# Kernel tuning notes

Measured on AMD Instinct MI355X. Metric: run time of the kernel, lower is better.

## Reference

```python
import jax, jax.numpy as jnp
import numpy as np

B, T, V, E, H, O = 32, 512, 32000, 512, 1024, 128


def setup_inputs() -> dict:
    key = jax.random.key(0)
    ks = jax.random.split(key, 8)
    s = lambda k, shape: (jax.random.normal(k, shape) * 0.02).astype(jnp.float32)
    return {
        "tokens": jax.random.randint(ks[0], (B, T), 0, V),
        "verb_indices": jax.random.randint(ks[1], (B,), 0, T),
        "emb": s(ks[2], (V, E)),
        "W_ih": s(ks[3], (4 * H, E)),
        "W_hh": s(ks[4], (4 * H, H)),
        "b_ih": jnp.zeros((4 * H,), jnp.float32),
        "b_hh": jnp.zeros((4 * H,), jnp.float32),
        "W_lin": s(ks[5], (O, 2 * H)),
        "b_lin": jnp.zeros((O,), jnp.float32),
    }


def _lstm(e, W_ih, W_hh, b_ih, b_hh):
    # e: [B,T,E] -> hidden states [B,T,H]; PyTorch gate order i,f,g,o
    Hd = W_hh.shape[1]
    # precompute input projections for all timesteps (one big GEMM)
    x_proj = jnp.einsum("bte,ge->btg", e, W_ih) + b_ih + b_hh  # [B,T,4H]

    def step(carry, x_t):
        h, c = carry
        gates = x_t + h @ W_hh.T  # [B,4H]
        i, f, g, o = jnp.split(gates, 4, axis=-1)
        i = jax.nn.sigmoid(i)
        f = jax.nn.sigmoid(f)
        g = jnp.tanh(g)
        o = jax.nn.sigmoid(o)
        c = f * c + i * g
        h = o * jnp.tanh(c)
        return (h, c), h

    h0 = jnp.zeros((e.shape[0], Hd), e.dtype)
    (_, _), hs = jax.lax.scan(step, (h0, h0), jnp.swapaxes(x_proj, 0, 1))
    return jnp.swapaxes(hs, 0, 1)  # [B,T,H]


def reference(tokens, verb_indices, emb, W_ih, W_hh, b_ih, b_hh, W_lin, b_lin):
    e = emb[tokens]  # [B,T,E]
    out = _lstm(e, W_ih, W_hh, b_ih, b_hh)  # [B,T,H]
    verbs = out[jnp.arange(out.shape[0]), verb_indices]  # [B,H] verb hidden state
    # linear over concat([verb, out_t]) == split the weight and sum two GEMMs
    Wv, Wo = jnp.split(W_lin, 2, axis=1)  # [O,H] each
    logits = (
        jnp.einsum("bh,oh->bo", verbs, Wv)[:, None, :]
        + jnp.einsum("bth,oh->bto", out, Wo)
        + b_lin
    )  # [B,T,O]
    return jax.nn.log_softmax(logits, axis=-1)
```

## Files before the change

### kernel.cpp

```cpp
#include <hip/hip_runtime.h>


typedef short s8v __attribute__((ext_vector_type(8)));
typedef float f4v __attribute__((ext_vector_type(4)));
typedef unsigned int u4v __attribute__((ext_vector_type(4)));

#define WS_CNT_OFF   131072
#define WS_VROWS_OFF 139264
#define WS_VLOG_OFF  204800

__device__ __forceinline__ float b2f(unsigned short u) {
    union { unsigned int i; float f; } x; x.i = ((unsigned int)u) << 16; return x.f;
}
__device__ __forceinline__ unsigned short f2b(float f) {
    union { float f; unsigned int i; } x; x.f = f;
    unsigned int r = (x.i + 0x7fffu + ((x.i >> 16) & 1u)) >> 16;
    return (unsigned short)r;
}
__device__ __forceinline__ float blo(unsigned int u) {
    union { unsigned int i; float f; } x; x.i = u << 16; return x.f;
}
__device__ __forceinline__ float bhi(unsigned int u) {
    union { unsigned int i; float f; } x; x.i = u & 0xffff0000u; return x.f;
}

__global__ void init_kernel(unsigned int* ws) {
    int i = blockIdx.x * 256 + threadIdx.x;
    if (i < 34816) ws[i] = 0u;
}

__device__ __forceinline__ void project_cols(
    const short* hA, const float* __restrict__ Wr0, const float* __restrict__ Wr1,
    float* __restrict__ dout, int b0, int tproj, int w, int tid)
{
    const int pair = tid >> 4, p = tid & 15;
    const int b = pair >> 1, oc = pair & 1;
    const float* wr = oc ? Wr1 : Wr0;
    float acc = 0.f;
#pragma unroll
    for (int j = 0; j < 8; ++j) {
        int ko = j * 16 + p;
        u4v d = *(const u4v*)&hA[(ko * 17 + b) * 8];
        const float* wk = wr + ko * 8;
        f4v w0 = *(const f4v*)wk, w1 = *(const f4v*)(wk + 4);
        unsigned int d0 = d[0], d1 = d[1], d2 = d[2], d3 = d[3];
        acc += blo(d0) * w0[0] + bhi(d0) * w0[1] + blo(d1) * w0[2] + bhi(d1) * w0[3]
             + blo(d2) * w1[0] + bhi(d2) * w1[1] + blo(d3) * w1[2] + bhi(d3) * w1[3];
    }
#pragma unroll
    for (int off = 1; off < 16; off <<= 1) acc += __shfl_xor(acc, off);
    if (p == 0)
        dout[((size_t)(b0 + b) * 512 + tproj) * 128 + 2 * w + oc] = acc;
}

__global__ __launch_bounds__(256, 1) void scan_kernel(
    const int* __restrict__ tokens,
    const int* __restrict__ vidx,
    const float* __restrict__ emb,
    const float* __restrict__ W_ih,
    const float* __restrict__ W_hh,
    const float* __restrict__ b_ih,
    const float* __restrict__ b_hh,
    const float* __restrict__ W_lin,
    unsigned short* __restrict__ hbuf,
    unsigned int* __restrict__ flags_all,
    unsigned short* __restrict__ vrows,
    float* __restrict__ dout)
{
    __shared__ short hA[128 * 17 * 8];
    __shared__ short eA[64 * 17 * 8];
    __shared__ float gbuf[16 * 65];

    const int tid  = threadIdx.x;
    const int g    = blockIdx.x >> 6;
    const int w    = blockIdx.x & 63;
    const int b0   = g * 8;
    const int lane = tid & 63;
    const int v    = tid >> 6;
    const int q    = lane >> 4;
    const int c    = lane & 15;

    const float* Wr0 = W_lin + (size_t)(2 * w) * 2048 + 1024;
    const float* Wr1 = W_lin + (size_t)(2 * w + 1) * 2048 + 1024;

    const int n = ((c >> 2) * 1024) + 16 * w + 4 * v + (c & 3);
    s8v Bh[32], Be[16];
    {
        const float* rh = W_hh + (size_t)n * 1024;
#pragma unroll
        for (int ks = 0; ks < 32; ++ks) {
            const float* s = rh + ks * 32 + q * 8;
            f4v lo = *(const f4v*)s, hi = *(const f4v*)(s + 4);
            s8v f;
#pragma unroll
            for (int j = 0; j < 4; ++j) { f[j] = (short)f2b(lo[j]); f[j + 4] = (short)f2b(hi[j]); }
            Bh[ks] = f;
        }
        const float* re = W_ih + (size_t)n * 512;
#pragma unroll
        for (int ks = 0; ks < 16; ++ks) {
            const float* s = re + ks * 32 + q * 8;
            f4v lo = *(const f4v*)s, hi = *(const f4v*)(s + 4);
            s8v f;
#pragma unroll
            for (int j = 0; j < 4; ++j) { f[j] = (short)f2b(lo[j]); f[j + 4] = (short)f2b(hi[j]); }
            Be[ks] = f;
        }
    }

    const s8v zv = {0,0,0,0,0,0,0,0};
    for (int i = tid; i < 1024; i += 256) { int ko = i >> 3, r = 8 + (i & 7);
        *(s8v*)&hA[(ko * 17 + r) * 8] = zv; }
    for (int i = tid; i < 512; i += 256) { int ko = i >> 3, r = 8 + (i & 7);
        *(s8v*)&eA[(ko * 17 + r) * 8] = zv; }

    float cst0 = 0.f, cst1 = 0.f;
    float bi0 = 0, bf0 = 0, bg0 = 0, bo0 = 0, bi1 = 0, bf1 = 0, bg1 = 0, bo1 = 0;
    int tvb = -1;
    const int pb = tid >> 3, pj2 = tid & 7;
    if (tid < 64) {
        int n0 = 16 * w + 2 * pj2, n1 = n0 + 1;
        bi0 = b_ih[n0]        + b_hh[n0];        bi1 = b_ih[n1]        + b_hh[n1];
        bf0 = b_ih[1024 + n0] + b_hh[1024 + n0]; bf1 = b_ih[1024 + n1] + b_hh[1024 + n1];
        bg0 = b_ih[2048 + n0] + b_hh[2048 + n0]; bg1 = b_ih[2048 + n1] + b_hh[2048 + n1];
        bo0 = b_ih[3072 + n0] + b_hh[3072 + n0]; bo1 = b_ih[3072 + n1] + b_hh[3072 + n1];
        tvb = vidx[b0 + pb];
    }

    unsigned short* hb   = hbuf + g * 2 * 8192;
    unsigned int*   hb32 = (unsigned int*)hb;
    unsigned int*   gflags = flags_all + g * 128;
    const int dwidx = ((2 * w + (pj2 >> 2)) * 8 + pb) * 4 + (pj2 & 3);
    int rp = 0;
    __syncthreads();

    for (int t = 0; t < 512; ++t) {
        for (int i = tid; i < 512; i += 256) {
            int ko = i >> 3, b = i & 7;
            int tok = tokens[(b0 + b) * 512 + t];
            const float* s = emb + (size_t)tok * 512 + ko * 8;
            f4v lo = *(const f4v*)s, hi = *(const f4v*)(s + 4);
            s8v f;
#pragma unroll
            for (int j = 0; j < 4; ++j) { f[j] = (short)f2b(lo[j]); f[j + 4] = (short)f2b(hi[j]); }
            *(s8v*)&eA[(ko * 17 + b) * 8] = f;
        }

        if (t >= 2)
            project_cols(hA, Wr0, Wr1, dout, b0, t - 2, w, tid);

        __syncthreads();

        f4v ae = {0.f, 0.f, 0.f, 0.f};
#pragma unroll
        for (int ks = 0; ks < 16; ++ks) {
            s8v a = *(const s8v*)&eA[((ks * 4 + q) * 17 + c) * 8];
            ae = __builtin_amdgcn_mfma_f32_16x16x32_bf16(a, Be[ks], ae, 0, 0, 0);
        }

        if (t > 0) {
            const unsigned tt = (unsigned)t;
            for (;;) {
                unsigned f = __hip_atomic_load(&gflags[lane], __ATOMIC_RELAXED,
                                               __HIP_MEMORY_SCOPE_AGENT);
                if (__all(f >= tt)) break;
            }
            asm volatile("" ::: "memory");
        }

        {
            const unsigned long long* src =
                (const unsigned long long*)(hb + rp * 8192);
#pragma unroll
            for (int it = 0; it < 8; ++it) {
                int j = it * 256 + tid;
                unsigned long long d = __hip_atomic_load(src + j, __ATOMIC_RELAXED,
                                                         __HIP_MEMORY_SCOPE_AGENT);
                int ko = j >> 4, b = (j >> 1) & 7, posq = (j & 1) << 2;
                *(unsigned long long*)&hA[(ko * 17 + b) * 8 + posq] = d;
            }
        }
        __syncthreads();

        f4v ah0 = {0.f, 0.f, 0.f, 0.f}, ah1 = {0.f, 0.f, 0.f, 0.f};
#pragma unroll
        for (int ks = 0; ks < 16; ++ks) {
            s8v a0 = *(const s8v*)&hA[((2 * ks) * 4 + q) * 17 * 8 + c * 8];
            s8v a1 = *(const s8v*)&hA[((2 * ks + 1) * 4 + q) * 17 * 8 + c * 8];
            ah0 = __builtin_amdgcn_mfma_f32_16x16x32_bf16(a0, Bh[2 * ks], ah0, 0, 0, 0);
            ah1 = __builtin_amdgcn_mfma_f32_16x16x32_bf16(a1, Bh[2 * ks + 1], ah1, 0, 0, 0);
        }

#pragma unroll
        for (int r = 0; r < 4; ++r)
            gbuf[(q * 4 + r) * 65 + v * 16 + c] = ae[r] + ah0[r] + ah1[r];
        __syncthreads();

        if (tid < 64) {
            float h0, h1;
            {
                int pj = 2 * pj2, base = (pj >> 2) * 16, cb = pj & 3;
                float xi = gbuf[pb * 65 + base + cb]      + bi0;
                float xf = gbuf[pb * 65 + base + 4 + cb]  + bf0;
                float xg = gbuf[pb * 65 + base + 8 + cb]  + bg0;
                float xo = gbuf[pb * 65 + base + 12 + cb] + bo0;
                float ig = 1.f / (1.f + __expf(-xi));
                float fg = 1.f / (1.f + __expf(-xf));
                float gg = 1.f - 2.f / (1.f + __expf(2.f * xg));
                float og = 1.f / (1.f + __expf(-xo));
                cst0 = fg * cst0 + ig * gg;
                h0 = og * (1.f - 2.f / (1.f + __expf(2.f * cst0)));
            }
            {
                int pj = 2 * pj2 + 1, base = (pj >> 2) * 16, cb = pj & 3;
                float xi = gbuf[pb * 65 + base + cb]      + bi1;
                float xf = gbuf[pb * 65 + base + 4 + cb]  + bf1;
                float xg = gbuf[pb * 65 + base + 8 + cb]  + bg1;
                float xo = gbuf[pb * 65 + base + 12 + cb] + bo1;
                float ig = 1.f / (1.f + __expf(-xi));
                float fg = 1.f / (1.f + __expf(-xf));
                float gg = 1.f - 2.f / (1.f + __expf(2.f * xg));
                float og = 1.f / (1.f + __expf(-xo));
                cst1 = fg * cst1 + ig * gg;
                h1 = og * (1.f - 2.f / (1.f + __expf(2.f * cst1)));
            }
            unsigned int pack = (unsigned int)f2b(h0) | ((unsigned int)f2b(h1) << 16);
            __hip_atomic_store(&hb32[(rp ^ 1) * 4096 + dwidx], pack,
                               __ATOMIC_RELAXED, __HIP_MEMORY_SCOPE_AGENT);
            if (t == tvb)
                *(unsigned int*)&vrows[(b0 + pb) * 1024 + 16 * w + 2 * pj2] = pack;
            asm volatile("s_waitcnt vmcnt(0)" ::: "memory");
            if (tid == 0)
                __hip_atomic_store(&gflags[w], (unsigned)(t + 1),
                                   __ATOMIC_RELAXED, __HIP_MEMORY_SCOPE_AGENT);
        }
        rp ^= 1;
    }

    project_cols(hA, Wr0, Wr1, dout, b0, 510, w, tid);
    __syncthreads();
    for (;;) {
        unsigned f = __hip_atomic_load(&gflags[lane], __ATOMIC_RELAXED,
                                       __HIP_MEMORY_SCOPE_AGENT);
        if (__all(f >= 512u)) break;
    }
    asm volatile("" ::: "memory");
    {
        const unsigned long long* src = (const unsigned long long*)(hb + rp * 8192);
#pragma unroll
        for (int it = 0; it < 8; ++it) {
            int j = it * 256 + tid;
            unsigned long long d = __hip_atomic_load(src + j, __ATOMIC_RELAXED,
                                                     __HIP_MEMORY_SCOPE_AGENT);
            int ko = j >> 4, b = (j >> 1) & 7, posq = (j & 1) << 2;
            *(unsigned long long*)&hA[(ko * 17 + b) * 8 + posq] = d;
        }
    }
    __syncthreads();
    project_cols(hA, Wr0, Wr1, dout, b0, 511, w, tid);
}

__global__ void verb_kernel(const unsigned short* __restrict__ vrows,
                            const float* __restrict__ W_lin,
                            const float* __restrict__ b_lin,
                            float* __restrict__ vlog)
{
    __shared__ float vrow[1024];
    int b = blockIdx.x, tid = threadIdx.x;
    for (int i = tid; i < 1024; i += 256) vrow[i] = b2f(vrows[b * 1024 + i]);
    __syncthreads();
    if (tid < 128) {
        float acc = 0.f;
        const float* wr = W_lin + (size_t)tid * 2048;
        for (int h = 0; h < 1024; ++h) acc += vrow[h] * wr[h];
        vlog[b * 128 + tid] = acc + b_lin[tid];
    }
}

__global__ void softmax_kernel(float* __restrict__ dout,
                               const float* __restrict__ vlog)
{
    int tid = threadIdx.x;
    int grow = blockIdx.x * 32 + (tid >> 3);
    int part = tid & 7;
    int b = grow >> 9;
    float* pp = dout + (size_t)grow * 128 + part * 16;
    const float* vb = vlog + b * 128 + part * 16;
    float L[16];
#pragma unroll
    for (int i = 0; i < 16; ++i) L[i] = pp[i] + vb[i];
    float m = L[0];
#pragma unroll
    for (int i = 1; i < 16; ++i) m = fmaxf(m, L[i]);
    for (int off = 1; off < 8; off <<= 1) m = fmaxf(m, __shfl_xor(m, off));
    float s = 0.f;
#pragma unroll
    for (int i = 0; i < 16; ++i) s += expf(L[i] - m);
    for (int off = 1; off < 8; off <<= 1) s += __shfl_xor(s, off);
    float lz = m + logf(s);
#pragma unroll
    for (int i = 0; i < 16; ++i) pp[i] = L[i] - lz;
}

extern "C" void kernel_launch(void* const* d_in, const int* in_sizes, int n_in,
                              void* d_out, int out_size, void* d_ws, size_t ws_size,
                              hipStream_t stream) {
    const int*   tokens = (const int*)d_in[0];
    const int*   vidx   = (const int*)d_in[1];
    const float* emb    = (const float*)d_in[2];
    const float* W_ih   = (const float*)d_in[3];
    const float* W_hh   = (const float*)d_in[4];
    const float* b_ih   = (const float*)d_in[5];
    const float* b_hh   = (const float*)d_in[6];
    const float* W_lin  = (const float*)d_in[7];
    const float* b_lin  = (const float*)d_in[8];
    float* dout = (float*)d_out;

    char* ws = (char*)d_ws;
    unsigned short* hbuf  = (unsigned short*)ws;
    unsigned int*   flags = (unsigned int*)(ws + WS_CNT_OFF);
    unsigned short* vrows = (unsigned short*)(ws + WS_VROWS_OFF);
    float*          vlog  = (float*)(ws + WS_VLOG_OFF);

    init_kernel<<<136, 256, 0, stream>>>((unsigned int*)ws);
    scan_kernel<<<256, 256, 0, stream>>>(tokens, vidx, emb, W_ih, W_hh, b_ih, b_hh,
                                         W_lin, hbuf, flags, vrows, dout);
    verb_kernel<<<32, 256, 0, stream>>>(vrows, W_lin, b_lin, vlog);
    softmax_kernel<<<512, 256, 0, stream>>>(dout, vlog);
}
```

Baseline: 3.548 ms.

## Fuse gate nonlinearity into all waves via shuffles and prefetch embeddings off critical path

```diff
diff --git a/kernel.cpp b/kernel.cpp
--- a/kernel.cpp
+++ b/kernel.cpp
@@ -68,8 +68,8 @@
     float* __restrict__ dout)
 {
     __shared__ short hA[128 * 17 * 8];
-    __shared__ short eA[64 * 17 * 8];
-    __shared__ float gbuf[16 * 65];
+    __shared__ short eA[2][64 * 17 * 8];
+    __shared__ int   tokL[512 * 8];
 
     const int tid  = threadIdx.x;
     const int g    = blockIdx.x >> 6;
@@ -108,62 +108,71 @@
         }
     }
 
+    for (int i = tid; i < 4096; i += 256)
+        tokL[(i & 511) * 8 + (i >> 9)] = tokens[(b0 + (i >> 9)) * 512 + (i & 511)];
+
     const s8v zv = {0,0,0,0,0,0,0,0};
     for (int i = tid; i < 1024; i += 256) { int ko = i >> 3, r = 8 + (i & 7);
         *(s8v*)&hA[(ko * 17 + r) * 8] = zv; }
     for (int i = tid; i < 512; i += 256) { int ko = i >> 3, r = 8 + (i & 7);
-        *(s8v*)&eA[(ko * 17 + r) * 8] = zv; }
-
-    float cst0 = 0.f, cst1 = 0.f;
-    float bi0 = 0, bf0 = 0, bg0 = 0, bo0 = 0, bi1 = 0, bf1 = 0, bg1 = 0, bo1 = 0;
-    int tvb = -1;
-    const int pb = tid >> 3, pj2 = tid & 7;
-    if (tid < 64) {
-        int n0 = 16 * w + 2 * pj2, n1 = n0 + 1;
-        bi0 = b_ih[n0]        + b_hh[n0];        bi1 = b_ih[n1]        + b_hh[n1];
-        bf0 = b_ih[1024 + n0] + b_hh[1024 + n0]; bf1 = b_ih[1024 + n1] + b_hh[1024 + n1];
-        bg0 = b_ih[2048 + n0] + b_hh[2048 + n0]; bg1 = b_ih[2048 + n1] + b_hh[2048 + n1];
-        bo0 = b_ih[3072 + n0] + b_hh[3072 + n0]; bo1 = b_ih[3072 + n1] + b_hh[3072 + n1];
-        tvb = vidx[b0 + pb];
-    }
-
-    unsigned short* hb   = hbuf + g * 2 * 8192;
-    unsigned int*   hb32 = (unsigned int*)hb;
-    unsigned int*   gflags = flags_all + g * 128;
-    const int dwidx = ((2 * w + (pj2 >> 2)) * 8 + pb) * 4 + (pj2 & 3);
+        *(s8v*)&eA[0][(ko * 17 + r) * 8] = zv;
+        *(s8v*)&eA[1][(ko * 17 + r) * 8] = zv; }
+    __syncthreads();
+
+    for (int i = tid; i < 512; i += 256) {
+        int ko = i >> 3, b = i & 7;
+        int tok = tokL[b];
+        const float* s = emb + (size_t)tok * 512 + ko * 8;
+        f4v lo = *(const f4v*)s, hi = *(const f4v*)(s + 4);
+        s8v f;
+#pragma unroll
+        for (int j = 0; j < 4; ++j) { f[j] = (short)f2b(lo[j]); f[j + 4] = (short)f2b(hi[j]); }
+        *(s8v*)&eA[0][(ko * 17 + b) * 8] = f;
+    }
+
+    const int jloc = 16 * w + 4 * v + (lane & 3);
+    const float bI = b_ih[jloc]        + b_hh[jloc];
+    const float bF = b_ih[1024 + jloc] + b_hh[1024 + jloc];
+    const float bG = b_ih[2048 + jloc] + b_hh[2048 + jloc];
+    const float bO = b_ih[3072 + jloc] + b_hh[3072 + jloc];
+    const int  shbase = (lane & 48) | (lane & 3);
+    const bool stAct  = ((lane & 12) == 0) && (lane < 32) && !(lane & 1);
+    const int  phid   = 8 * w + 2 * v + ((lane >> 1) & 1);
+    const int  Db     = (phid >> 2) * 32 + (phid & 3) + (lane >> 4) * 16;
+    int tv0 = -1, tv1 = -1, tv2 = -1, tv3 = -1;
+    if (stAct) {
+        int bb = b0 + 4 * (lane >> 4);
+        tv0 = vidx[bb]; tv1 = vidx[bb + 1]; tv2 = vidx[bb + 2]; tv3 = vidx[bb + 3];
+    }
+    const int vrb = (b0 + 4 * (lane >> 4)) * 1024 + jloc;
+
+    float cst[4] = {0.f, 0.f, 0.f, 0.f};
+    unsigned short* hb     = hbuf + g * 2 * 8192;
+    unsigned int*   hb32   = (unsigned int*)hb;
+    unsigned int*   gflags = flags_all + g * 256;
     int rp = 0;
     __syncthreads();
 
     for (int t = 0; t < 512; ++t) {
-        for (int i = tid; i < 512; i += 256) {
-            int ko = i >> 3, b = i & 7;
-            int tok = tokens[(b0 + b) * 512 + t];
-            const float* s = emb + (size_t)tok * 512 + ko * 8;
-            f4v lo = *(const f4v*)s, hi = *(const f4v*)(s + 4);
-            s8v f;
-#pragma unroll
-            for (int j = 0; j < 4; ++j) { f[j] = (short)f2b(lo[j]); f[j + 4] = (short)f2b(hi[j]); }
-            *(s8v*)&eA[(ko * 17 + b) * 8] = f;
-        }
-
-        if (t >= 2)
-            project_cols(hA, Wr0, Wr1, dout, b0, t - 2, w, tid);
-
-        __syncthreads();
-
         f4v ae = {0.f, 0.f, 0.f, 0.f};
+        const short* eAc = eA[t & 1];
 #pragma unroll
         for (int ks = 0; ks < 16; ++ks) {
-            s8v a = *(const s8v*)&eA[((ks * 4 + q) * 17 + c) * 8];
+            s8v a = *(const s8v*)&eAc[((ks * 4 + q) * 17 + c) * 8];
             ae = __builtin_amdgcn_mfma_f32_16x16x32_bf16(a, Be[ks], ae, 0, 0, 0);
         }
 
         if (t > 0) {
             const unsigned tt = (unsigned)t;
             for (;;) {
-                unsigned f = __hip_atomic_load(&gflags[lane], __ATOMIC_RELAXED,
-                                               __HIP_MEMORY_SCOPE_AGENT);
-                if (__all(f >= tt)) break;
+                unsigned f0 = __hip_atomic_load(&gflags[lane],       __ATOMIC_RELAXED, __HIP_MEMORY_SCOPE_AGENT);
+                unsigned f1 = __hip_atomic_load(&gflags[64 + lane],  __ATOMIC_RELAXED, __HIP_MEMORY_SCOPE_AGENT);
+                unsigned f2 = __hip_atomic_load(&gflags[128 + lane], __ATOMIC_RELAXED, __HIP_MEMORY_SCOPE_AGENT);
+                unsigned f3 = __hip_atomic_load(&gflags[192 + lane], __ATOMIC_RELAXED, __HIP_MEMORY_SCOPE_AGENT);
+                unsigned m01 = f0 < f1 ? f0 : f1;
+                unsigned m23 = f2 < f3 ? f2 : f3;
+                unsigned m = m01 < m23 ? m01 : m23;
+                if (__all(m >= tt)) break;
             }
             asm volatile("" ::: "memory");
         }
@@ -191,58 +200,69 @@
             ah1 = __builtin_amdgcn_mfma_f32_16x16x32_bf16(a1, Bh[2 * ks + 1], ah1, 0, 0, 0);
         }
 
-#pragma unroll
-        for (int r = 0; r < 4; ++r)
-            gbuf[(q * 4 + r) * 65 + v * 16 + c] = ae[r] + ah0[r] + ah1[r];
+        int hui[4];
+#pragma unroll
+        for (int r = 0; r < 4; ++r) {
+            float s = ae[r] + ah0[r] + ah1[r];
+            float xi = __shfl(s, shbase);
+            float xf = __shfl(s, shbase + 4);
+            float xg = __shfl(s, shbase + 8);
+            float xo = __shfl(s, shbase + 12);
+            float ig = 1.f / (1.f + __expf(-(xi + bI)));
+            float fg = 1.f / (1.f + __expf(-(xf + bF)));
+            float gg = 1.f - 2.f / (1.f + __expf(2.f * (xg + bG)));
+            float og = 1.f / (1.f + __expf(-(xo + bO)));
+            cst[r] = fg * cst[r] + ig * gg;
+            float h = og * (1.f - 2.f / (1.f + __expf(2.f * cst[r])));
+            hui[r] = (int)f2b(h);
+        }
+#pragma unroll
+        for (int r = 0; r < 4; ++r) {
+            int ph = __shfl_xor(hui[r], 1);
+            if (stAct) {
+                unsigned pack = (unsigned)hui[r] | (((unsigned)ph) << 16);
+                __hip_atomic_store(&hb32[(rp ^ 1) * 4096 + Db + r * 4], pack,
+                                   __ATOMIC_RELAXED, __HIP_MEMORY_SCOPE_AGENT);
+                int tvr = (r == 0) ? tv0 : (r == 1) ? tv1 : (r == 2) ? tv2 : tv3;
+                if (t == tvr)
+                    *(unsigned int*)&vrows[vrb + r * 1024] = pack;
+            }
+        }
+        asm volatile("s_waitcnt vmcnt(0)" ::: "memory");
+        if (lane == 0)
+            __hip_atomic_store(&gflags[w * 4 + v], (unsigned)(t + 1),
+                               __ATOMIC_RELAXED, __HIP_MEMORY_SCOPE_AGENT);
+
+        if (t >= 1)
+            project_cols(hA, Wr0, Wr1, dout, b0, t - 1, w, tid);
+
+        if (t < 511) {
+            int tn = t + 1;
+            short* eAn = eA[tn & 1];
+            for (int i = tid; i < 512; i += 256) {
+                int ko = i >> 3, b = i & 7;
+                int tok = tokL[tn * 8 + b];
+                const float* s2 = emb + (size_t)tok * 512 + ko * 8;
+                f4v lo = *(const f4v*)s2, hi = *(const f4v*)(s2 + 4);
+                s8v f;
+#pragma unroll
+                for (int j2 = 0; j2 < 4; ++j2) { f[j2] = (short)f2b(lo[j2]); f[j2 + 4] = (short)f2b(hi[j2]); }
+                *(s8v*)&eAn[(ko * 17 + b) * 8] = f;
+            }
+        }
         __syncthreads();
-
-        if (tid < 64) {
-            float h0, h1;
-            {
-                int pj = 2 * pj2, base = (pj >> 2) * 16, cb = pj & 3;
-                float xi = gbuf[pb * 65 + base + cb]      + bi0;
-                float xf = gbuf[pb * 65 + base + 4 + cb]  + bf0;
-                float xg = gbuf[pb * 65 + base + 8 + cb]  + bg0;
-                float xo = gbuf[pb * 65 + base + 12 + cb] + bo0;
-                float ig = 1.f / (1.f + __expf(-xi));
-                float fg = 1.f / (1.f + __expf(-xf));
-                float gg = 1.f - 2.f / (1.f + __expf(2.f * xg));
-                float og = 1.f / (1.f + __expf(-xo));
-                cst0 = fg * cst0 + ig * gg;
-                h0 = og * (1.f - 2.f / (1.f + __expf(2.f * cst0)));
-            }
-            {
-                int pj = 2 * pj2 + 1, base = (pj >> 2) * 16, cb = pj & 3;
-                float xi = gbuf[pb * 65 + base + cb]      + bi1;
-                float xf = gbuf[pb * 65 + base + 4 + cb]  + bf1;
-                float xg = gbuf[pb * 65 + base + 8 + cb]  + bg1;
-                float xo = gbuf[pb * 65 + base + 12 + cb] + bo1;
-                float ig = 1.f / (1.f + __expf(-xi));
-                float fg = 1.f / (1.f + __expf(-xf));
-                float gg = 1.f - 2.f / (1.f + __expf(2.f * xg));
-                float og = 1.f / (1.f + __expf(-xo));
-                cst1 = fg * cst1 + ig * gg;
-                h1 = og * (1.f - 2.f / (1.f + __expf(2.f * cst1)));
-            }
-            unsigned int pack = (unsigned int)f2b(h0) | ((unsigned int)f2b(h1) << 16);
-            __hip_atomic_store(&hb32[(rp ^ 1) * 4096 + dwidx], pack,
-                               __ATOMIC_RELAXED, __HIP_MEMORY_SCOPE_AGENT);
-            if (t == tvb)
-                *(unsigned int*)&vrows[(b0 + pb) * 1024 + 16 * w + 2 * pj2] = pack;
-            asm volatile("s_waitcnt vmcnt(0)" ::: "memory");
-            if (tid == 0)
-                __hip_atomic_store(&gflags[w], (unsigned)(t + 1),
-                                   __ATOMIC_RELAXED, __HIP_MEMORY_SCOPE_AGENT);
-        }
         rp ^= 1;
     }
 
-    project_cols(hA, Wr0, Wr1, dout, b0, 510, w, tid);
-    __syncthreads();
     for (;;) {
-        unsigned f = __hip_atomic_load(&gflags[lane], __ATOMIC_RELAXED,
-                                       __HIP_MEMORY_SCOPE_AGENT);
-        if (__all(f >= 512u)) break;
+        unsigned f0 = __hip_atomic_load(&gflags[lane],       __ATOMIC_RELAXED, __HIP_MEMORY_SCOPE_AGENT);
+        unsigned f1 = __hip_atomic_load(&gflags[64 + lane],  __ATOMIC_RELAXED, __HIP_MEMORY_SCOPE_AGENT);
+        unsigned f2 = __hip_atomic_load(&gflags[128 + lane], __ATOMIC_RELAXED, __HIP_MEMORY_SCOPE_AGENT);
+        unsigned f3 = __hip_atomic_load(&gflags[192 + lane], __ATOMIC_RELAXED, __HIP_MEMORY_SCOPE_AGENT);
+        unsigned m01 = f0 < f1 ? f0 : f1;
+        unsigned m23 = f2 < f3 ? f2 : f3;
+        unsigned m = m01 < m23 ? m01 : m23;
+        if (__all(m >= 512u)) break;
     }
     asm volatile("" ::: "memory");
     {
```

Measured after the change: 3.800 ms. 7.1% more time.
